# Kernel optimization log

Measured on AMD Instinct MI355X. Metric: run time of the kernel, lower is better.

## Reference

```python
import jax, jax.numpy as jnp
import numpy as np

N_NODES = 10000
N_EDGES = 320000
N_GRAPHS = 64
L = 3  # num_layers


def _gru(a, h, wih, whh, bih, bhh):
    # torch.nn.GRUCell math: input a, hidden h
    gi = a @ wih.T + bih
    gh = h @ whh.T + bhh
    ir, iz, inn = jnp.split(gi, 3, axis=-1)
    hr, hz, hn = jnp.split(gh, 3, axis=-1)
    r = jax.nn.sigmoid(ir + hr)
    z = jax.nn.sigmoid(iz + hz)
    n = jnp.tanh(inn + r * hn)
    return (1.0 - z) * n + z * h


def _ggc(x, src, dst, w, wih, whh, bih, bhh):
    # PyG GatedGraphConv: pad features up to out_channels, then L rounds of
    # (linear -> scatter-add over edges -> GRUCell update)
    out_ch = w.shape[-1]
    if x.shape[-1] < out_ch:
        x = jnp.concatenate(
            [x, jnp.zeros((x.shape[0], out_ch - x.shape[-1]), x.dtype)], axis=-1)
    for i in range(w.shape[0]):
        m = x @ w[i]                                        # [N, C]
        a = jax.ops.segment_sum(m[src], dst, num_segments=N_NODES)  # scatter-add
        x = _gru(a, x, wih, whh, bih, bhh)
    return x


def setup_inputs() -> dict:
    key = jax.random.key(0)
    ks = jax.random.split(key, 16)
    d1, d2 = 128, 256
    s1, s2 = 1.0 / np.sqrt(d1), 1.0 / np.sqrt(d2)
    x = jax.random.normal(ks[0], (N_NODES, d1), dtype=jnp.float32)
    edge_index = jax.random.randint(ks[1], (2, N_EDGES), 0, N_NODES, dtype=jnp.int64)
    batch = jnp.sort(jax.random.randint(ks[2], (N_NODES,), 0, N_GRAPHS, dtype=jnp.int64))
    return {
        "x": x,
        "edge_index": edge_index,
        "batch": batch,
        "w1": jax.random.normal(ks[3], (L, d1, d1), jnp.float32) * s1,
        "gru1_wih": jax.random.normal(ks[4], (3 * d1, d1), jnp.float32) * s1,
        "gru1_whh": jax.random.normal(ks[5], (3 * d1, d1), jnp.float32) * s1,
        "gru1_bih": jax.random.normal(ks[6], (3 * d1,), jnp.float32) * s1,
        "gru1_bhh": jax.random.normal(ks[7], (3 * d1,), jnp.float32) * s1,
        "w2": jax.random.normal(ks[8], (L, d2, d2), jnp.float32) * s2,
        "gru2_wih": jax.random.normal(ks[9], (3 * d2, d2), jnp.float32) * s2,
        "gru2_whh": jax.random.normal(ks[10], (3 * d2, d2), jnp.float32) * s2,
        "gru2_bih": jax.random.normal(ks[11], (3 * d2,), jnp.float32) * s2,
        "gru2_bhh": jax.random.normal(ks[12], (3 * d2,), jnp.float32) * s2,
        "fc_w": jax.random.normal(ks[13], (6, d2), jnp.float32) * s2,
        "fc_b": jnp.zeros((6,), jnp.float32),
    }


def reference(x, edge_index, batch, w1, gru1_wih, gru1_whh, gru1_bih, gru1_bhh,
              w2, gru2_wih, gru2_whh, gru2_bih, gru2_bhh, fc_w, fc_b):
    src, dst = edge_index[0], edge_index[1]
    y = jax.nn.relu(_ggc(x, src, dst, w1, gru1_wih, gru1_whh, gru1_bih, gru1_bhh))
    y = _ggc(y, src, dst, w2, gru2_wih, gru2_whh, gru2_bih, gru2_bhh)
    y = jax.ops.segment_max(y, batch, num_segments=N_GRAPHS)  # global max pool [G, 256]
    return y @ fc_w.T + fc_b  # [G, 6]
```

## Files before the change

### kernel.cpp

```cpp
#include <hip/hip_runtime.h>

#define NN 10000
#define NNP 10112
#define NE 320000
#define NG 64
#define D1 128
#define D2 256
#define MT 158

typedef unsigned short u16;
typedef short v8s __attribute__((ext_vector_type(8)));
typedef float v4f __attribute__((ext_vector_type(4)));

__device__ __forceinline__ u16 f2bf(float x) {
    unsigned u = __float_as_uint(x);
    return (u16)((u + 0x7fffu + ((u >> 16) & 1u)) >> 16);
}
__device__ __forceinline__ float bf2f(u16 b) {
    return __uint_as_float(((unsigned)b) << 16);
}
__device__ __forceinline__ float sigm(float x) { return 1.f / (1.f + __expf(-x)); }
__device__ __forceinline__ float tanh_f(float x) {
    float cx = fminf(fmaxf(x, -15.f), 15.f);
    float e = __expf(2.f * cx);
    return (e - 1.f) / (e + 1.f);
}

#define MF(d, a, b) d = __builtin_amdgcn_mfma_f32_16x16x32_bf16(a, b, d, 0, 0, 0)

#define SWZ(bx, by)                              \
    const int bid_ = blockIdx.x;                 \
    const int l_ = bid_ >> 3;                    \
    const int by = (bid_ & 7) * 20 + l_ % 20;    \
    const int bx = l_ / 20;                      \
    if (by >= MT) return;


template<int C, int MODE, int OS>
__global__ __launch_bounds__(256, 2)
void giqru_k(const u16* __restrict__ Ah, const u16* __restrict__ Al,
             const u16* __restrict__ Xh, const u16* __restrict__ Xl,
             const u16* __restrict__ WcH, const u16* __restrict__ WcL,
             const float* __restrict__ bih, const float* __restrict__ bhh,
             u16* __restrict__ xh_out, u16* __restrict__ xl_out,
             float* __restrict__ xf_out,
             const int* __restrict__ batch, unsigned* __restrict__ pool) {
    SWZ(bx, by)
    const int tid = threadIdx.x;
    const int wave = tid >> 6, lane = tid & 63;
    const int bm = by * 64;
    const int quad = lane >> 4, r16 = lane & 15;
    constexpr int K2 = 2 * C;
    constexpr int NK = K2 >> 5;
    constexpr int CCH = C >> 3;
    const size_t arow = (size_t)by * CCH;
    const size_t wtile = (size_t)(bx * 2 + (wave >> 1)) * (K2 >> 3);
    const int aoff = r16 * 8;
    const int woff = ((wave & 1) * 64 + r16) * 8;

    v4f acc[4][4] = {};
#pragma unroll
    for (int ks = 0; ks < NK; ++ks) {
        const int k0 = ks << 5;
        const bool ap = k0 < C;
        const int kk = ap ? k0 : k0 - C;
        const u16* sh = ap ? Ah : Xh;
        const u16* sl = ap ? Al : Xl;
        const size_t ach = (arow + (kk >> 3) + quad) * 512;
        const size_t wch = (wtile + (k0 >> 3) + quad) * 1024;
        const int g2 = ap ? 2 : 3;
        v8s fah[4], fal[4], wh[3], wl[3];
#pragma unroll
        for (int i = 0; i < 4; ++i) {
            fah[i] = *(const v8s*)(Ah + 0, sh + ach + aoff + i * 128);
            fal[i] = *(const v8s*)(sl + ach + aoff + i * 128);
        }
        wh[0] = *(const v8s*)(WcH + wch + woff);
        wl[0] = *(const v8s*)(WcL + wch + woff);
        wh[1] = *(const v8s*)(WcH + wch + woff + 128);
        wl[1] = *(const v8s*)(WcL + wch + woff + 128);
        wh[2] = *(const v8s*)(WcH + wch + woff + g2 * 128);
        wl[2] = *(const v8s*)(WcL + wch + woff + g2 * 128);
#pragma unroll
        for (int i = 0; i < 4; ++i) {
            MF(acc[i][0], fah[i], wh[0]); MF(acc[i][0], fah[i], wl[0]); MF(acc[i][0], fal[i], wh[0]);
            MF(acc[i][1], fah[i], wh[1]); MF(acc[i][1], fah[i], wl[1]); MF(acc[i][1], fal[i], wh[1]);
            if (ap) {
                MF(acc[i][2], fah[i], wh[2]); MF(acc[i][2], fah[i], wl[2]); MF(acc[i][2], fal[i], wh[2]);
            } else {
                MF(acc[i][3], fah[i], wh[2]); MF(acc[i][3], fah[i], wl[2]); MF(acc[i][3], fal[i], wh[2]);
            }
        }
    }

    const int c = (bx * 4 + wave) * 16 + r16;
    const float br = bih[c] + bhh[c];
    const float bz = bih[C + c] + bhh[C + c];
    const float bi_n = bih[2 * C + c];
    const float bh_n = bhh[2 * C + c];
    const int cch = c >> 3, cr = c & 7;
#pragma unroll
    for (int i = 0; i < 4; ++i) {
        int R0 = bm + i * 16 + quad * 4;
#pragma unroll
        for (int r = 0; r < 4; ++r) {
            int R = R0 + r;
            if (R >= NN) continue;
            float rr = sigm(acc[i][0][r] + br);
            float zz = sigm(acc[i][1][r] + bz);
            float nn_ = tanh_f(acc[i][2][r] + bi_n + rr * (acc[i][3][r] + bh_n));
            size_t hx = ((size_t)(R >> 6) * CCH + cch) * 512 + ((R & 63) << 3) + cr;
            float h = bf2f(Xh[hx]) + bf2f(Xl[hx]);
            float o = (1.f - zz) * nn_ + zz * h;
            if (MODE == 2) {
                unsigned b = __float_as_uint(o);
                unsigned u = (b & 0x80000000u) ? ~b : (b | 0x80000000u);
                atomicMax(&pool[batch[R] * 256 + c], u);
            } else {
                if (MODE == 1) o = fmaxf(o, 0.f);
                size_t ox = ((size_t)(R >> 6) * (OS >> 3) + cch) * 512 + ((R & 63) << 3) + cr;
                u16 hh = f2bf(o);
                xh_out[ox] = hh;
                xl_out[ox] = f2bf(o - bf2f(hh));
                xf_out[(size_t)R * OS + c] = o;
            }
        }
    }
}

__global__ void count_k(const int* __restrict__ dst, int* __restrict__ cnt) {
    int e = blockIdx.x * blockDim.x + threadIdx.x;
    if (e < NE) atomicAdd(&cnt[dst[e]], 1);
}

__global__ void scan_k(const int* __restrict__ cnt, int* __restrict__ off,
                       int* __restrict__ cur) {
    __shared__ int ps[1024];
    const int tid = threadIdx.x;
    const int CH = (NN + 1023) / 1024;
    const int base = tid * CH;
    int s = 0;
    for (int i = 0; i < CH; ++i) {
        int idx = base + i;
        if (idx < NN) s += cnt[idx];
    }
    ps[tid] = s;
    __syncthreads();
    for (int d = 1; d < 1024; d <<= 1) {
        int v = (tid >= d) ? ps[tid - d] : 0;
        __syncthreads();
        ps[tid] += v;
        __syncthreads();
    }
    int run = (tid > 0) ? ps[tid - 1] : 0;
    for (int i = 0; i < CH; ++i) {
        int idx = base + i;
        if (idx <= NN) { off[idx] = run; if (idx < NN) cur[idx] = run; }
        if (idx < NN) run += cnt[idx];
    }
}

__global__ void fill_k(const int* __restrict__ src, const int* __restrict__ dst,
                       int* __restrict__ cur, int* __restrict__ elist) {
    int e = blockIdx.x * blockDim.x + threadIdx.x;
    if (e >= NE) return;
    int p = atomicAdd(&cur[dst[e]], 1);
    elist[p] = src[e];
}

template<int C>
__global__ void gather_k(const float* __restrict__ xf, const int* __restrict__ off,
                         const int* __restrict__ elist,
                         u16* __restrict__ ah, u16* __restrict__ al) {
    constexpr int LPN = C / 4;
    const int GB = gridDim.x;
    const int q = GB >> 3, r = GB & 7;
    const int xx = blockIdx.x & 7, oo = blockIdx.x >> 3;
    const int wg = (xx < r ? xx * (q + 1) : r * (q + 1) + (xx - r) * q) + oo;
    int t = wg * 256 + threadIdx.x;
    int node = t / LPN;
    if (node >= NN) return;
    int c = (t % LPN) * 4;
    int s0 = off[node], s1 = off[node + 1];
    v4f a0 = 0.f, a1 = 0.f, a2 = 0.f, a3 = 0.f;
    int i = s0;
    for (; i + 4 <= s1; i += 4) {
        int e0 = elist[i], e1 = elist[i + 1], e2 = elist[i + 2], e3 = elist[i + 3];
        v4f v0 = *(const v4f*)(xf + (size_t)e0 * C + c);
        v4f v1 = *(const v4f*)(xf + (size_t)e1 * C + c);
        v4f v2 = *(const v4f*)(xf + (size_t)e2 * C + c);
        v4f v3 = *(const v4f*)(xf + (size_t)e3 * C + c);
        a0 += v0; a1 += v1; a2 += v2; a3 += v3;
    }
    for (; i < s1; ++i) {
        int e = elist[i];
        a0 += *(const v4f*)(xf + (size_t)e * C + c);
    }
    v4f acc = (a0 + a1) + (a2 + a3);
    ushort4 h, l;
    h.x = f2bf(acc[0]); l.x = f2bf(acc[0] - bf2f(h.x));
    h.y = f2bf(acc[1]); l.y = f2bf(acc[1] - bf2f(h.y));
    h.z = f2bf(acc[2]); l.z = f2bf(acc[2] - bf2f(h.z));
    h.w = f2bf(acc[3]); l.w = f2bf(acc[3] - bf2f(h.w));
    size_t ox = ((size_t)(node >> 6) * (C >> 3) + (c >> 3)) * 512 + ((node & 63) << 3) + (c & 7);
    *(ushort4*)(ah + ox) = h;
    *(ushort4*)(al + ox) = l;
}

__global__ void weff_k(const float* __restrict__ w, const float* __restrict__ wih,
                       u16* __restrict__ WcH, u16* __restrict__ WcL, int C) {
    __shared__ float As[64 * 65];
    __shared__ float Bs[64 * 65];
    const int k0 = blockIdx.x * 64, jp0 = blockIdx.y * 64, it = blockIdx.z;
    const int tid = threadIdx.x;
    const int tx = tid & 15, ty = tid >> 4;
    const int K2 = 2 * C;
    float acc[4][4] = {};
    for (int j0 = 0; j0 < C; j0 += 64) {
        for (int idx = tid; idx < 4096; idx += 256) {
            int row = idx >> 6, j = idx & 63;
            As[row * 65 + j] = w[((size_t)it * C + k0 + row) * C + j0 + j];
            int jp = jp0 + row;
            int cc = ((jp >> 6) << 4) | (jp & 15);
            int g = (jp >> 4) & 3;
            Bs[row * 65 + j] = (g < 3) ? wih[((size_t)g * C + cc) * C + j0 + j] : 0.f;
        }
        __syncthreads();
        for (int j = 0; j < 64; ++j) {
            float a0 = As[(tx * 4 + 0) * 65 + j];
            float a1 = As[(tx * 4 + 1) * 65 + j];
            float a2 = As[(tx * 4 + 2) * 65 + j];
            float a3 = As[(tx * 4 + 3) * 65 + j];
            float b0 = Bs[(ty * 4 + 0) * 65 + j];
            float b1 = Bs[(ty * 4 + 1) * 65 + j];
            float b2 = Bs[(ty * 4 + 2) * 65 + j];
            float b3 = Bs[(ty * 4 + 3) * 65 + j];
            acc[0][0] += b0 * a0; acc[0][1] += b0 * a1; acc[0][2] += b0 * a2; acc[0][3] += b0 * a3;
            acc[1][0] += b1 * a0; acc[1][1] += b1 * a1; acc[1][2] += b1 * a2; acc[1][3] += b1 * a3;
            acc[2][0] += b2 * a0; acc[2][1] += b2 * a1; acc[2][2] += b2 * a2; acc[2][3] += b2 * a3;
            acc[3][0] += b3 * a0; acc[3][1] += b3 * a1; acc[3][2] += b3 * a2; acc[3][3] += b3 * a3;
        }
        __syncthreads();
    }
    const size_t its = (size_t)it * 8 * C * C;
#pragma unroll
    for (int a = 0; a < 4; ++a) {
        int jp = jp0 + ty * 4 + a;
#pragma unroll
        for (int b = 0; b < 4; ++b) {
            int k = k0 + tx * 4 + b;
            float v = acc[a][b];
            u16 h = f2bf(v);
            size_t o = its + ((size_t)(jp >> 7) * (K2 >> 3) + (k >> 3)) * 1024 + ((jp & 127) << 3) + (k & 7);
            WcH[o] = h;
            WcL[o] = f2bf(v - bf2f(h));
        }
    }
}

__global__ void prep_k(const float* __restrict__ whh1, const float* __restrict__ whh2,
                       const float* __restrict__ xin,
                       u16* __restrict__ Wc1h, u16* __restrict__ Wc1l,
                       u16* __restrict__ Wc2h, u16* __restrict__ Wc2l,
                       u16* __restrict__ xh, u16* __restrict__ xl) {
    const int q1 = 3 * 512 * 128;
    const int q2 = 3 * 1024 * 256;
    int t = blockIdx.x * blockDim.x + threadIdx.x;
    if (t < q1) {
        int it = t / (512 * 128), r = t - it * (512 * 128);
        int jp = r >> 7, kk = r & 127;
        int c = ((jp >> 6) << 4) | (jp & 15);
        int g = (jp >> 4) & 3;
        float v = (g == 0) ? whh1[c * D1 + kk]
                : (g == 1) ? whh1[(D1 + c) * D1 + kk]
                : (g == 2) ? 0.f
                           : whh1[(2 * D1 + c) * D1 + kk];
        int k = D1 + kk;
        u16 h = f2bf(v);
        size_t o = (size_t)it * 131072 + ((size_t)(jp >> 7) * 32 + (k >> 3)) * 1024 + ((jp & 127) << 3) + (k & 7);
        Wc1h[o] = h; Wc1l[o] = f2bf(v - bf2f(h)); return;
    }
    t -= q1;
    if (t < q2) {
        int it = t / (1024 * 256), r = t - it * (1024 * 256);
        int jp = r >> 8, kk = r & 255;
        int c = ((jp >> 6) << 4) | (jp & 15);
        int g = (jp >> 4) & 3;
        float v = (g == 0) ? whh2[c * D2 + kk]
                : (g == 1) ? whh2[(D2 + c) * D2 + kk]
                : (g == 2) ? 0.f
                           : whh2[(2 * D2 + c) * D2 + kk];
        int k = D2 + kk;
        u16 h = f2bf(v);
        size_t o = (size_t)it * 524288 + ((size_t)(jp >> 7) * 64 + (k >> 3)) * 1024 + ((jp & 127) << 3) + (k & 7);
        Wc2h[o] = h; Wc2l[o] = f2bf(v - bf2f(h)); return;
    }
    t -= q2;
    if (t < NN * D1) {
        int n = t >> 7, cc = t & 127;
        float v = xin[t];
        u16 h = f2bf(v);
        size_t o = ((size_t)(n >> 6) * 16 + (cc >> 3)) * 512 + ((n & 63) << 3) + (cc & 7);
        xh[o] = h;
        xl[o] = f2bf(v - bf2f(h));
    }
}

__global__ void pad_k(u16* __restrict__ xh, u16* __restrict__ xl,
                      float* __restrict__ xf) {
    int t = blockIdx.x * blockDim.x + threadIdx.x;
    if (t >= NNP * 128) return;
    int n = t >> 7, c = 128 + (t & 127);
    size_t o = ((size_t)(n >> 6) * 32 + (c >> 3)) * 512 + ((n & 63) << 3) + (c & 7);
    xh[o] = 0;
    xl[o] = 0;
    xf[(size_t)n * 256 + c] = 0.f;
}

__global__ void pool_init_k(unsigned* __restrict__ pool) {
    int t = blockIdx.x * blockDim.x + threadIdx.x;
    if (t < NG * D2) pool[t] = 0x007FFFFFu;
}

__global__ void fc_k(const unsigned* __restrict__ pool, const float* __restrict__ w,
                     const float* __restrict__ b, float* __restrict__ out) {
    int t = blockIdx.x * blockDim.x + threadIdx.x;
    if (t >= NG * 6) return;
    int g = t / 6, o = t - g * 6;
    float s = b[o];
    for (int c = 0; c < D2; ++c) {
        unsigned u = pool[g * D2 + c];
        unsigned bits = (u & 0x80000000u) ? (u ^ 0x80000000u) : ~u;
        s += __uint_as_float(bits) * w[o * D2 + c];
    }
    out[t] = s;
}

extern "C" void kernel_launch(void* const* d_in, const int* in_sizes, int n_in,
                              void* d_out, int out_size, void* d_ws, size_t ws_size,
                              hipStream_t stream) {
    const float* x_in = (const float*)d_in[0];
    const int* ei = (const int*)d_in[1];
    const int* src = ei;
    const int* dst = ei + NE;
    const int* batch = (const int*)d_in[2];
    const float* w1   = (const float*)d_in[3];
    const float* wih1 = (const float*)d_in[4];
    const float* whh1 = (const float*)d_in[5];
    const float* bih1 = (const float*)d_in[6];
    const float* bhh1 = (const float*)d_in[7];
    const float* w2   = (const float*)d_in[8];
    const float* wih2 = (const float*)d_in[9];
    const float* whh2 = (const float*)d_in[10];
    const float* bih2 = (const float*)d_in[11];
    const float* bhh2 = (const float*)d_in[12];
    const float* fcw  = (const float*)d_in[13];
    const float* fcb  = (const float*)d_in[14];
    float* out = (float*)d_out;

    u16* a_h  = (u16*)d_ws;
    u16* a_l  = a_h + (size_t)NNP * 256;
    u16* xA0h = a_l + (size_t)NNP * 256;
    u16* xA0l = xA0h + (size_t)NNP * 128;
    u16* xA1h = xA0l + (size_t)NNP * 128;
    u16* xA1l = xA1h + (size_t)NNP * 128;
    u16* xB0h = xA1l + (size_t)NNP * 128;
    u16* xB0l = xB0h + (size_t)NNP * 256;
    u16* xB1h = xB0l + (size_t)NNP * 256;
    u16* xB1l = xB1h + (size_t)NNP * 256;
    u16* Wc1h = xB1l + (size_t)NNP * 256;
    u16* Wc1l = Wc1h + (size_t)3 * 512 * 256;
    u16* Wc2h = Wc1l + (size_t)3 * 512 * 256;
    u16* Wc2l = Wc2h + (size_t)3 * 1024 * 512;
    float* xfA = (float*)(Wc2l + (size_t)3 * 1024 * 512);
    float* xfB = xfA + (size_t)NNP * 128;
    int* cnt   = (int*)(xfB + (size_t)NNP * 256);
    int* off   = cnt + NN;
    int* cur   = off + NN + 1;
    int* elist = cur + NN;
    unsigned* pool = (unsigned*)(elist + NE);

    hipMemsetAsync(cnt, 0, NN * sizeof(int), stream);
    count_k<<<(NE + 255) / 256, 256, 0, stream>>>(dst, cnt);
    scan_k<<<1, 1024, 0, stream>>>(cnt, off, cur);
    fill_k<<<(NE + 255) / 256, 256, 0, stream>>>(src, dst, cur, elist);
    {
        int total = 3 * 512 * 128 + 3 * 1024 * 256 + NN * D1;
        prep_k<<<(total + 255) / 256, 256, 0, stream>>>(
            whh1, whh2, x_in, Wc1h, Wc1l, Wc2h, Wc2l, xA0h, xA0l);
    }
    weff_k<<<dim3(D1 / 64, 4 * D1 / 64, 3), 256, 0, stream>>>(w1, wih1, Wc1h, Wc1l, D1);
    weff_k<<<dim3(D2 / 64, 4 * D2 / 64, 3), 256, 0, stream>>>(w2, wih2, Wc2h, Wc2l, D2);
    pad_k<<<(NNP * 128 + 255) / 256, 256, 0, stream>>>(xB0h, xB0l, xfB);
    pool_init_k<<<(NG * D2 + 255) / 256, 256, 0, stream>>>(pool);

    const int G1 = 160 * 2;
    const int G2 = 160 * 4;
    const int GG1 = (NN * (D1 / 4) + 255) / 256;
    const int GG2 = (NN * (D2 / 4) + 255) / 256;
    const size_t W1S = 131072, W2S = 524288;

    gather_k<D1><<<GG1, 256, 0, stream>>>(x_in, off, elist, a_h, a_l);
    giqru_k<D1, 0, 128><<<G1, 256, 0, stream>>>(
        a_h, a_l, xA0h, xA0l, Wc1h, Wc1l, bih1, bhh1,
        xA1h, xA1l, xfA, nullptr, nullptr);

    gather_k<D1><<<GG1, 256, 0, stream>>>(xfA, off, elist, a_h, a_l);
    giqru_k<D1, 0, 128><<<G1, 256, 0, stream>>>(
        a_h, a_l, xA1h, xA1l, Wc1h + W1S, Wc1l + W1S, bih1, bhh1,
        xA0h, xA0l, xfA, nullptr, nullptr);

    gather_k<D1><<<GG1, 256, 0, stream>>>(xfA, off, elist, a_h, a_l);
    giqru_k<D1, 1, 256><<<G1, 256, 0, stream>>>(
        a_h, a_l, xA0h, xA0l, Wc1h + 2 * W1S, Wc1l + 2 * W1S, bih1, bhh1,
        xB0h, xB0l, xfB, nullptr, nullptr);

    gather_k<D2><<<GG2, 256, 0, stream>>>(xfB, off, elist, a_h, a_l);
    giqru_k<D2, 0, 256><<<G2, 256, 0, stream>>>(
        a_h, a_l, xB0h, xB0l, Wc2h, Wc2l, bih2, bhh2,
        xB1h, xB1l, xfB, nullptr, nullptr);

    gather_k<D2><<<GG2, 256, 0, stream>>>(xfB, off, elist, a_h, a_l);
    giqru_k<D2, 0, 256><<<G2, 256, 0, stream>>>(
        a_h, a_l, xB1h, xB1l, Wc2h + W2S, Wc2l + W2S, bih2, bhh2,
        xB0h, xB0l, xfB, nullptr, nullptr);

    gather_k<D2><<<GG2, 256, 0, stream>>>(xfB, off, elist, a_h, a_l);
    giqru_k<D2, 2, 256><<<G2, 256, 0, stream>>>(
        a_h, a_l, xB0h, xB0l, Wc2h + 2 * W2S, Wc2l + 2 * W2S, bih2, bhh2,
        nullptr, nullptr, nullptr, batch, pool);

    fc_k<<<1, 512, 0, stream>>>(pool, fcw, fcb, out);
}
```

Baseline: 584.8 us.

## Stage GEMM tiles in LDS via global_load_lds with 128-row block tiles

The fused GRU GEMM kernel now stages each K-slice of the A/X and weight tiles into shared memory with direct global-to-LDS loads. Each block covers 128 rows instead of 64, and the 2x2 wave arrangement shares both A rows and weight columns across waves. The block-to-tile mapping is replaced with a new XCD-aware scheme, occupancy is raised to 3 blocks per SM, and the gather kernel drops its block swizzle. The aim is to cut redundant global loads of A and weights, at the cost of two barriers per K step and no double buffering.

```diff
diff --git a/kernel.cpp b/kernel.cpp
--- a/kernel.cpp
+++ b/kernel.cpp
@@ -6,7 +6,7 @@
 #define NG 64
 #define D1 128
 #define D2 256
-#define MT 158
+#define MT128 79
 
 typedef unsigned short u16;
 typedef short v8s __attribute__((ext_vector_type(8)));
@@ -28,16 +28,14 @@
 
 #define MF(d, a, b) d = __builtin_amdgcn_mfma_f32_16x16x32_bf16(a, b, d, 0, 0, 0)
 
-#define SWZ(bx, by)                              \
-    const int bid_ = blockIdx.x;                 \
-    const int l_ = bid_ >> 3;                    \
-    const int by = (bid_ & 7) * 20 + l_ % 20;    \
-    const int bx = l_ / 20;                      \
-    if (by >= MT) return;
-
-
-template<int C, int MODE, int OS>
-__global__ __launch_bounds__(256, 2)
+#define GLDS16(gp, lp)                                                         \
+    __builtin_amdgcn_global_load_lds(                                          \
+        (__attribute__((address_space(1))) unsigned int*)(unsigned long long)(gp), \
+        (__attribute__((address_space(3))) unsigned int*)(lp), 16, 0, 0)
+
+
+template<int C, int MODE, int OS, int RP>
+__global__ __launch_bounds__(256, 3)
 void giqru_k(const u16* __restrict__ Ah, const u16* __restrict__ Al,
              const u16* __restrict__ Xh, const u16* __restrict__ Xl,
              const u16* __restrict__ WcH, const u16* __restrict__ WcL,
@@ -45,55 +43,73 @@
              u16* __restrict__ xh_out, u16* __restrict__ xl_out,
              float* __restrict__ xf_out,
              const int* __restrict__ batch, unsigned* __restrict__ pool) {
-    SWZ(bx, by)
+    const int bid = blockIdx.x;
+    const int px = (bid & 7) / RP;
+    const int byt = (bid >> 3) * RP + ((bid & 7) % RP);
+    if (byt >= MT128) return;
+    __shared__ u16 lds[16384];
     const int tid = threadIdx.x;
     const int wave = tid >> 6, lane = tid & 63;
-    const int bm = by * 64;
+    const int wr = wave >> 1, wc = wave & 1;
     const int quad = lane >> 4, r16 = lane & 15;
+    const int bm = byt * 128;
     constexpr int K2 = 2 * C;
     constexpr int NK = K2 >> 5;
     constexpr int CCH = C >> 3;
-    const size_t arow = (size_t)by * CCH;
-    const size_t wtile = (size_t)(bx * 2 + (wave >> 1)) * (K2 >> 3);
-    const int aoff = r16 * 8;
-    const int woff = ((wave & 1) * 64 + r16) * 8;
+    const size_t art = (size_t)(byt * 2);
+    const size_t wrow = (size_t)px * (K2 >> 3);
 
     v4f acc[4][4] = {};
-#pragma unroll
     for (int ks = 0; ks < NK; ++ks) {
         const int k0 = ks << 5;
         const bool ap = k0 < C;
-        const int kk = ap ? k0 : k0 - C;
         const u16* sh = ap ? Ah : Xh;
         const u16* sl = ap ? Al : Xl;
-        const size_t ach = (arow + (kk >> 3) + quad) * 512;
-        const size_t wch = (wtile + (k0 >> 3) + quad) * 1024;
+        const int kc = (ap ? k0 : k0 - C) >> 3;
+#pragma unroll
+        for (int s2 = 0; s2 < 8; ++s2) {
+            int u = s2 * 4 + wave;
+            const u16* gp; int ld;
+            if (u < 8)       { int t = u >> 2, q = u & 3;
+                gp = sh + ((art + t) * CCH + kc + q) * 512;            ld = q * 1024 + t * 512; }
+            else if (u < 16) { int v = u - 8; int t = v >> 2, q = v & 3;
+                gp = sl + ((art + t) * CCH + kc + q) * 512;            ld = 4096 + q * 1024 + t * 512; }
+            else if (u < 24) { int v = u - 16; int q = v >> 1, h = v & 1;
+                gp = WcH + (wrow + (k0 >> 3) + q) * 1024 + h * 512;    ld = 8192 + q * 1024 + h * 512; }
+            else             { int v = u - 24; int q = v >> 1, h = v & 1;
+                gp = WcL + (wrow + (k0 >> 3) + q) * 1024 + h * 512;    ld = 12288 + q * 1024 + h * 512; }
+            GLDS16(gp + lane * 8, &lds[ld]);
+        }
+        __syncthreads();
+        v8s fah[4], fal[4];
+#pragma unroll
+        for (int i = 0; i < 4; ++i) {
+            int ra = (quad * 128 + wr * 64 + i * 16 + r16) * 8;
+            fah[i] = *(const v8s*)&lds[ra];
+            fal[i] = *(const v8s*)&lds[4096 + ra];
+        }
         const int g2 = ap ? 2 : 3;
-        v8s fah[4], fal[4], wh[3], wl[3];
+        const int p0 = 8192 + (quad * 128 + wc * 64 + r16) * 8;
+        v8s w0h = *(const v8s*)&lds[p0];
+        v8s w0l = *(const v8s*)&lds[4096 + p0];
+        v8s w1h = *(const v8s*)&lds[p0 + 128];
+        v8s w1l = *(const v8s*)&lds[4096 + p0 + 128];
+        v8s w2h = *(const v8s*)&lds[p0 + g2 * 128];
+        v8s w2l = *(const v8s*)&lds[4096 + p0 + g2 * 128];
 #pragma unroll
         for (int i = 0; i < 4; ++i) {
-            fah[i] = *(const v8s*)(Ah + 0, sh + ach + aoff + i * 128);
-            fal[i] = *(const v8s*)(sl + ach + aoff + i * 128);
-        }
-        wh[0] = *(const v8s*)(WcH + wch + woff);
-        wl[0] = *(const v8s*)(WcL + wch + woff);
-        wh[1] = *(const v8s*)(WcH + wch + woff + 128);
-        wl[1] = *(const v8s*)(WcL + wch + woff + 128);
-        wh[2] = *(const v8s*)(WcH + wch + woff + g2 * 128);
-        wl[2] = *(const v8s*)(WcL + wch + woff + g2 * 128);
-#pragma unroll
-        for (int i = 0; i < 4; ++i) {
-            MF(acc[i][0], fah[i], wh[0]); MF(acc[i][0], fah[i], wl[0]); MF(acc[i][0], fal[i], wh[0]);
-            MF(acc[i][1], fah[i], wh[1]); MF(acc[i][1], fah[i], wl[1]); MF(acc[i][1], fal[i], wh[1]);
+            MF(acc[i][0], fah[i], w0h); MF(acc[i][0], fah[i], w0l); MF(acc[i][0], fal[i], w0h);
+            MF(acc[i][1], fah[i], w1h); MF(acc[i][1], fah[i], w1l); MF(acc[i][1], fal[i], w1h);
             if (ap) {
-                MF(acc[i][2], fah[i], wh[2]); MF(acc[i][2], fah[i], wl[2]); MF(acc[i][2], fal[i], wh[2]);
+                MF(acc[i][2], fah[i], w2h); MF(acc[i][2], fah[i], w2l); MF(acc[i][2], fal[i], w2h);
             } else {
-                MF(acc[i][3], fah[i], wh[2]); MF(acc[i][3], fah[i], wl[2]); MF(acc[i][3], fal[i], wh[2]);
+                MF(acc[i][3], fah[i], w2h); MF(acc[i][3], fah[i], w2l); MF(acc[i][3], fal[i], w2h);
             }
         }
-    }
-
-    const int c = (bx * 4 + wave) * 16 + r16;
+        __syncthreads();
+    }
+
+    const int c = px * 32 + wc * 16 + r16;
     const float br = bih[c] + bhh[c];
     const float bz = bih[C + c] + bhh[C + c];
     const float bi_n = bih[2 * C + c];
@@ -101,7 +117,7 @@
     const int cch = c >> 3, cr = c & 7;
 #pragma unroll
     for (int i = 0; i < 4; ++i) {
-        int R0 = bm + i * 16 + quad * 4;
+        int R0 = bm + wr * 64 + i * 16 + quad * 4;
 #pragma unroll
         for (int r = 0; r < 4; ++r) {
             int R = R0 + r;
@@ -173,11 +189,7 @@
                          const int* __restrict__ elist,
                          u16* __restrict__ ah, u16* __restrict__ al) {
     constexpr int LPN = C / 4;
-    const int GB = gridDim.x;
-    const int q = GB >> 3, r = GB & 7;
-    const int xx = blockIdx.x & 7, oo = blockIdx.x >> 3;
-    const int wg = (xx < r ? xx * (q + 1) : r * (q + 1) + (xx - r) * q) + oo;
-    int t = wg * 256 + threadIdx.x;
+    int t = blockIdx.x * blockDim.x + threadIdx.x;
     int node = t / LPN;
     if (node >= NN) return;
     int c = (t % LPN) * 4;
@@ -394,39 +406,39 @@
     pad_k<<<(NNP * 128 + 255) / 256, 256, 0, stream>>>(xB0h, xB0l, xfB);
     pool_init_k<<<(NG * D2 + 255) / 256, 256, 0, stream>>>(pool);
 
-    const int G1 = 160 * 2;
-    const int G2 = 160 * 4;
+    const int G1 = 8 * 40;
+    const int G2 = 8 * 79;
     const int GG1 = (NN * (D1 / 4) + 255) / 256;
     const int GG2 = (NN * (D2 / 4) + 255) / 256;
     const size_t W1S = 131072, W2S = 524288;
 
     gather_k<D1><<<GG1, 256, 0, stream>>>(x_in, off, elist, a_h, a_l);
-    giqru_k<D1, 0, 128><<<G1, 256, 0, stream>>>(
+    giqru_k<D1, 0, 128, 2><<<G1, 256, 0, stream>>>(
         a_h, a_l, xA0h, xA0l, Wc1h, Wc1l, bih1, bhh1,
         xA1h, xA1l, xfA, nullptr, nullptr);
 
     gather_k<D1><<<GG1, 256, 0, stream>>>(xfA, off, elist, a_h, a_l);
-    giqru_k<D1, 0, 128><<<G1, 256, 0, stream>>>(
+    giqru_k<D1, 0, 128, 2><<<G1, 256, 0, stream>>>(
         a_h, a_l, xA1h, xA1l, Wc1h + W1S, Wc1l + W1S, bih1, bhh1,
         xA0h, xA0l, xfA, nullptr, nullptr);
 
     gather_k<D1><<<GG1, 256, 0, stream>>>(xfA, off, elist, a_h, a_l);
-    giqru_k<D1, 1, 256><<<G1, 256, 0, stream>>>(
+    giqru_k<D1, 1, 256, 2><<<G1, 256, 0, stream>>>(
         a_h, a_l, xA0h, xA0l, Wc1h + 2 * W1S, Wc1l + 2 * W1S, bih1, bhh1,
         xB0h, xB0l, xfB, nullptr, nullptr);
 
     gather_k<D2><<<GG2, 256, 0, stream>>>(xfB, off, elist, a_h, a_l);
-    giqru_k<D2, 0, 256><<<G2, 256, 0, stream>>>(
+    giqru_k<D2, 0, 256, 1><<<G2, 256, 0, stream>>>(
         a_h, a_l, xB0h, xB0l, Wc2h, Wc2l, bih2, bhh2,
         xB1h, xB1l, xfB, nullptr, nullptr);
 
     gather_k<D2><<<GG2, 256, 0, stream>>>(xfB, off, elist, a_h, a_l);
-    giqru_k<D2, 0, 256><<<G2, 256, 0, stream>>>(
+    giqru_k<D2, 0, 256, 1><<<G2, 256, 0, stream>>>(
         a_h, a_l, xB1h, xB1l, Wc2h + W2S, Wc2l + W2S, bih2, bhh2,
         xB0h, xB0l, xfB, nullptr, nullptr);
 
     gather_k<D2><<<GG2, 256, 0, stream>>>(xfB, off, elist, a_h, a_l);
-    giqru_k<D2, 2, 256><<<G2, 256, 0, stream>>>(
+    giqru_k<D2, 2, 256, 1><<<G2, 256, 0, stream>>>(
         a_h, a_l, xB0h, xB0l, Wc2h + 2 * W2S, Wc2l + 2 * W2S, bih2, bhh2,
         nullptr, nullptr, nullptr, batch, pool);
 
```

New measurement: 621.0 us. +6.2%, slower.
